# Performance work log

Hardware: AMD Instinct MI355X
Metric: run time of the kernel (lower is better)

The kernel has to match this reference:

```python
import jax, jax.numpy as jnp
import numpy as np

# db2 decomposition filters (pywt values); pytorch_wavelets reverses them and uses
# F.conv1d (cross-correlation), so we store the reversed filters.
_DEC_LO = np.array([-0.12940952255092145, 0.22414386804185735,
                    0.836516303737469, 0.48296291314469025])
_DEC_HI = np.array([-0.48296291314469025, 0.836516303737469,
                    -0.22414386804185735, 0.12940952255092145])
_H0 = jnp.asarray(_DEC_LO[::-1].copy(), dtype=jnp.float32)
_H1 = jnp.asarray(_DEC_HI[::-1].copy(), dtype=jnp.float32)


def _dwt_layer(x):
    """Vectorized equivalent of DWTLayer: db2 J=1 DWT along the channel axis at
    every (b,i,j) pixel, keeping first C//2 lo coeffs then first C//2 hi coeffs.
    pytorch_wavelets mode='zero' with L=4 and even C -> pad 2 each side, stride 2.
    x: [B, C, H, W] -> [B, C, H, W]
    """
    B, C, H, W = x.shape
    v = jnp.transpose(x, (0, 2, 3, 1)).reshape(B * H * W, 1, C)
    filt = jnp.stack([_H0, _H1])[:, None, :].astype(x.dtype)  # [2,1,4]
    out = jax.lax.conv_general_dilated(
        v, filt, window_strides=(2,), padding=((2, 2),),
        dimension_numbers=('NCH', 'OIH', 'NCH'))  # [BHW, 2, C//2 + 1]
    half = C // 2
    t = jnp.concatenate([out[:, 0, :half], out[:, 1, :half]], axis=-1)
    return jnp.transpose(t.reshape(B, H, W, C), (0, 3, 1, 2))


def setup_inputs() -> dict:
    key = jax.random.key(0)
    ks = jax.random.split(key, 7)
    B, C, H, W = 16, 360, 64, 64
    return {
        'x': jax.random.normal(ks[0], (B, C, H, W), dtype=jnp.float32),
        'conv_w': jax.random.normal(ks[1], (1, 1, 2, 7), dtype=jnp.float32) * 0.1,
        'conv_b': jax.random.normal(ks[2], (1,), dtype=jnp.float32) * 0.1,
        'w1': jax.random.normal(ks[3], (128, 90), dtype=jnp.float32) * 0.1,
        'b1': jax.random.normal(ks[4], (128,), dtype=jnp.float32) * 0.1,
        'w2': jax.random.normal(ks[5], (256, 128), dtype=jnp.float32) * 0.1,
        'b2': jax.random.normal(ks[6], (256,), dtype=jnp.float32) * 0.1,
    }


def reference(x, conv_w, conv_b, w1, b1, w2, b2):
    x = _dwt_layer(x)                     # [B,360,H,W]
    cd1 = x[:, 180:, :, :]                # detail half -> [B,180,H,W]
    cd1 = _dwt_layer(cd1)                 # [B,180,H,W]
    cd1 = cd1.reshape(-1, 1, 2, 90)       # torch .view(-1,2,90).unsqueeze(1)
    cd1 = jax.lax.conv_general_dilated(
        cd1, conv_w, window_strides=(1, 1), padding=((0, 0), (3, 3)),
        dimension_numbers=('NCHW', 'OIHW', 'NCHW'))
    cd1 = cd1 + conv_b[None, :, None, None]   # [N,1,1,90]
    cd1 = jax.nn.relu(cd1)
    cd1 = cd1.reshape(cd1.shape[0], 1, -1)    # [N,1,90]
    cd1 = jax.nn.relu(cd1 @ w1.T + b1)        # [N,1,128]
    out = cd1 @ w2.T + b2                     # [N,1,256]
    return out.reshape(-1, 256, 8, 8)
```

## Files before the change

kernel.cpp:

```cpp
#include <hip/hip_runtime.h>

using bf8   = __attribute__((ext_vector_type(8))) short;
using f32x4 = __attribute__((ext_vector_type(4))) float;

__device__ inline unsigned short f2bf(float f) {
  unsigned u = __float_as_uint(f);
  return (unsigned short)((u + 0x7FFFu + ((u >> 16) & 1u)) >> 16);
}
__device__ inline float bf2f(unsigned short h) {
  return __uint_as_float(((unsigned)h) << 16);
}

struct Gs { float g0[10]; float g1[10]; };
__host__ __device__ constexpr Gs make_g() {
  double H0[4] = {0.48296291314469025, 0.836516303737469,
                  0.22414386804185735, -0.12940952255092145};
  double H1[4] = {0.12940952255092145, -0.22414386804185735,
                  0.836516303737469, -0.48296291314469025};
  Gs r{};
  for (int d = 0; d < 10; ++d) {
    double a = 0.0, b = 0.0;
    for (int k = 0; k < 4; ++k) {
      int j = d - 2 * k;
      if (j >= 0 && j < 4) { a += H0[k] * H1[j]; b += H1[k] * H1[j]; }
    }
    r.g0[d] = (float)a; r.g1[d] = (float)b;
  }
  return r;
}

__global__ __launch_bounds__(256) void dwt2_kernel(const float* __restrict__ x,
                                                   unsigned short* __restrict__ A) {
  constexpr Gs G = make_g();
  const int bx    = blockIdx.x;
  const int seg   = bx & 7;
  const int pb    = bx >> 3;
  const int b     = pb >> 2;
  const int chunk = pb & 3;
  const int s     = chunk * 1024 + 4 * threadIdx.x;

  const float4* xb = (const float4*)(x + (size_t)b * 360 * 4096 + s);
  unsigned short* Ab = A + (size_t)b * 180 * 4096 + s;

  const int c0 = (seg * 90) >> 3;
  const int c1 = ((seg + 1) * 90) >> 3;

  float4 w[10];
  const int base = 4 * c0 - 6;
#pragma unroll
  for (int i = 0; i < 10; ++i) {
    const int idx = base + i;
    w[i] = (idx >= 0) ? xb[(size_t)idx * 1024] : float4{0.f, 0.f, 0.f, 0.f};
  }

  for (int c = c0; c < c1; ++c) {
    float4 nx[4];
    const bool pf = (c + 1 < c1);
    const int nb = 4 * c + 4;
#pragma unroll
    for (int i = 0; i < 4; ++i)
      nx[i] = pf ? xb[(size_t)(nb + i) * 1024] : float4{0.f, 0.f, 0.f, 0.f};

    float4 lo{0.f, 0.f, 0.f, 0.f}, hi{0.f, 0.f, 0.f, 0.f};
#pragma unroll
    for (int d = 0; d < 10; ++d) {
      lo.x = fmaf(G.g0[d], w[d].x, lo.x);
      lo.y = fmaf(G.g0[d], w[d].y, lo.y);
      lo.z = fmaf(G.g0[d], w[d].z, lo.z);
      lo.w = fmaf(G.g0[d], w[d].w, lo.w);
      hi.x = fmaf(G.g1[d], w[d].x, hi.x);
      hi.y = fmaf(G.g1[d], w[d].y, hi.y);
      hi.z = fmaf(G.g1[d], w[d].z, hi.z);
      hi.w = fmaf(G.g1[d], w[d].w, hi.w);
    }
    *(ushort4*)&Ab[(size_t)c * 4096] =
        ushort4{f2bf(lo.x), f2bf(lo.y), f2bf(lo.z), f2bf(lo.w)};
    *(ushort4*)&Ab[(size_t)(c + 90) * 4096] =
        ushort4{f2bf(hi.x), f2bf(hi.y), f2bf(hi.z), f2bf(hi.w)};
#pragma unroll
    for (int i = 0; i < 6; ++i) w[i] = w[i + 4];
#pragma unroll
    for (int i = 0; i < 4; ++i) w[6 + i] = nx[i];
  }
}

__global__ __launch_bounds__(256) void conv_kernel(
    const unsigned short* __restrict__ A,
    const float* __restrict__ cw, const float* __restrict__ cb,
    unsigned short* __restrict__ Y,
    const float* __restrict__ w1, const float* __restrict__ w2,
    unsigned short* __restrict__ w1b, unsigned short* __restrict__ w2b) {
  const int bx = blockIdx.x;
  if (bx >= 1024) {
    const int e = bx - 1024;
#pragma unroll
    for (int t = 0; t < 4; ++t) {
      const int i = e * 1024 + t * 256 + threadIdx.x;
      if (i < 13312) {
        const int o = i / 104, k = i - 104 * o;
        w1b[i] = (k < 90) ? f2bf(w1[o * 90 + k]) : (unsigned short)0;
      } else {
        const int j = i - 13312;
        const int o = j / 136, k = j - 136 * o;
        w2b[j] = (k < 128) ? f2bf(w2[o * 128 + k]) : (unsigned short)0;
      }
    }
    return;
  }

  __shared__ float As[64 * 180];
  const int tid = threadIdx.x;
  const size_t g0 = (size_t)bx * 64;

  const uint4* src = (const uint4*)(A + g0 * 180);
  for (int i = tid; i < 1440; i += 256) {
    uint4 v = src[i];
    float* d = &As[8 * i];
    d[0] = bf2f((unsigned short)(v.x & 0xFFFF));
    d[1] = bf2f((unsigned short)(v.x >> 16));
    d[2] = bf2f((unsigned short)(v.y & 0xFFFF));
    d[3] = bf2f((unsigned short)(v.y >> 16));
    d[4] = bf2f((unsigned short)(v.z & 0xFFFF));
    d[5] = bf2f((unsigned short)(v.z >> 16));
    d[6] = bf2f((unsigned short)(v.w & 0xFFFF));
    d[7] = bf2f((unsigned short)(v.w >> 16));
  }
  __syncthreads();

  float cwr[14];
#pragma unroll
  for (int k = 0; k < 14; ++k) cwr[k] = cw[k];
  const float cbv = cb[0];

  for (int i = tid; i < 64 * 24; i += 256) {
    const int g = i / 24, j4 = i - g * 24, j0 = 4 * j4;
    const float* Ag = &As[g * 180];
    float v0[10], v1[10];
#pragma unroll
    for (int t = 0; t < 10; ++t) {
      const int m = j0 - 3 + t;
      const bool ok = (m >= 0) && (m < 90);
      v0[t] = ok ? Ag[m] : 0.0f;
      v1[t] = ok ? Ag[90 + m] : 0.0f;
    }
    ushort4 o4;
    unsigned short* op = (unsigned short*)&o4;
#pragma unroll
    for (int d = 0; d < 4; ++d) {
      const int j = j0 + d;
      float acc = 0.0f;
      if (j < 90) {
        acc = cbv;
#pragma unroll
        for (int k = 0; k < 7; ++k) {
          acc = fmaf(v0[d + k], cwr[k], acc);
          acc = fmaf(v1[d + k], cwr[7 + k], acc);
        }
        acc = fmaxf(acc, 0.0f);
      }
      op[d] = f2bf(acc);
    }
    *(ushort4*)&Y[(g0 + g) * 96 + j0] = o4;
  }
}

__global__ __launch_bounds__(256) void mlp_mfma_kernel(
    const unsigned short* __restrict__ Y,
    const unsigned short* __restrict__ w1b,
    const unsigned short* __restrict__ w2b,
    const float* __restrict__ b1, const float* __restrict__ b2,
    float* __restrict__ out) {
  __shared__ unsigned short w1B[128 * 104];
  __shared__ unsigned short w2B[128 * 136];
  __shared__ unsigned short HY[64 * 136];
  __shared__ float bias[256];

  const int tid = threadIdx.x;
  const int fam = blockIdx.x & 1;
  const int cb  = blockIdx.x >> 1;

  {
    const uint4* s1 = (const uint4*)w1b;
    for (int i = tid; i < 1664; i += 256) ((uint4*)w1B)[i] = s1[i];
    const uint4* s2 = (const uint4*)(w2b + (size_t)fam * 128 * 136);
    for (int i = tid; i < 2176; i += 256) ((uint4*)w2B)[i] = s2[i];
    bias[tid] = (tid < 128) ? b1[tid] : b2[fam * 128 + (tid - 128)];
  }

  const int w = tid >> 6, lane = tid & 63;
  const int l15 = lane & 15, q = lane >> 4;
  const int mrow = 16 * w + l15;

  for (int it = 0; it < 4; ++it) {
    const size_t g0 = (size_t)(cb + 256 * it) * 64;

    __syncthreads();

    const uint4* ys = (const uint4*)(Y + g0 * 96);
    for (int i = tid; i < 768; i += 256) {
      const int r = i / 12, c = i - 12 * r;
      *(uint4*)&HY[r * 104 + 8 * c] = ys[i];
    }
    __syncthreads();

    bf8 ya[3];
#pragma unroll
    for (int ks = 0; ks < 3; ++ks)
      ya[ks] = *(const bf8*)&HY[mrow * 104 + 32 * ks + 8 * q];

    f32x4 acc1[8];
#pragma unroll
    for (int nt = 0; nt < 8; ++nt) {
      f32x4 a = {0.f, 0.f, 0.f, 0.f};
#pragma unroll
      for (int ks = 0; ks < 3; ++ks) {
        const bf8 wb = *(const bf8*)&w1B[(16 * nt + l15) * 104 + 32 * ks + 8 * q];
        a = __builtin_amdgcn_mfma_f32_16x16x32_bf16(ya[ks], wb, a, 0, 0, 0);
      }
      acc1[nt] = a;
    }
    __syncthreads();

#pragma unroll
    for (int nt = 0; nt < 8; ++nt) {
#pragma unroll
      for (int r = 0; r < 4; ++r) {
        const int n = 16 * w + 4 * q + r;
        const int o = 16 * nt + l15;
        HY[n * 136 + o] = f2bf(fmaxf(acc1[nt][r] + bias[o], 0.0f));
      }
    }
    __syncthreads();

    bf8 ha[4];
#pragma unroll
    for (int ks = 0; ks < 4; ++ks)
      ha[ks] = *(const bf8*)&HY[mrow * 136 + 32 * ks + 8 * q];

#pragma unroll 2
    for (int nt = 0; nt < 8; ++nt) {
      f32x4 a = {0.f, 0.f, 0.f, 0.f};
#pragma unroll
      for (int ks = 0; ks < 4; ++ks) {
        const bf8 wb = *(const bf8*)&w2B[(16 * nt + l15) * 136 + 32 * ks + 8 * q];
        a = __builtin_amdgcn_mfma_f32_16x16x32_bf16(ha[ks], wb, a, 0, 0, 0);
      }
#pragma unroll
      for (int r = 0; r < 4; ++r) {
        const int n = 16 * w + 4 * q + r;
        const int o = 16 * nt + l15;
        out[(g0 + n) * 256 + fam * 128 + o] = a[r] + bias[128 + o];
      }
    }
  }
}

extern "C" void kernel_launch(void* const* d_in, const int* in_sizes, int n_in,
                              void* d_out, int out_size, void* d_ws, size_t ws_size,
                              hipStream_t stream) {
  const float* x  = (const float*)d_in[0];
  const float* cw = (const float*)d_in[1];
  const float* cb = (const float*)d_in[2];
  const float* w1 = (const float*)d_in[3];
  const float* b1 = (const float*)d_in[4];
  const float* w2 = (const float*)d_in[5];
  const float* b2 = (const float*)d_in[6];
  float* outp = (float*)d_out;

  unsigned short* Abf = (unsigned short*)d_ws;
  unsigned short* Ybf = Abf + (size_t)16 * 180 * 4096;
  unsigned short* w1b = Ybf + (size_t)65536 * 96;
  unsigned short* w2b = w1b + 13312;

  dwt2_kernel<<<512, 256, 0, stream>>>(x, Abf);
  conv_kernel<<<1071, 256, 0, stream>>>(Abf, cw, cb, Ybf, w1, w2, w1b, w2b);
  mlp_mfma_kernel<<<512, 256, 0, stream>>>(Ybf, w1b, w2b, b1, b2, outp);
}
```

Before: 206.6 us.

## Fuse conv into MLP kernel and move weight conversion into DWT launch

Removes the separate conv kernel by computing the 2x7 conv+ReLU on the fly inside the MLP kernel, building MFMA A-fragments directly from bf16 DWT output staged in shared memory. Weight bf16 conversion moves into extra blocks of the DWT launch, so three launches become two and the Y intermediate buffer is no longer written or read. The MLP kernel now uses 512-thread blocks handling 128 rows, register-prefetches the next tile from global memory, and keeps biases in registers. The risks are higher register pressure, scalar bf16 LDS reads for the conv taps, and fewer blocks (256), which could lower occupancy.

```diff
diff --git a/kernel.cpp b/kernel.cpp
--- a/kernel.cpp
+++ b/kernel.cpp
@@ -30,9 +30,30 @@
 }
 
 __global__ __launch_bounds__(256) void dwt2_kernel(const float* __restrict__ x,
-                                                   unsigned short* __restrict__ A) {
+                                                   unsigned short* __restrict__ A,
+                                                   const float* __restrict__ w1,
+                                                   const float* __restrict__ w2,
+                                                   unsigned short* __restrict__ w1b,
+                                                   unsigned short* __restrict__ w2b) {
   constexpr Gs G = make_g();
-  const int bx    = blockIdx.x;
+  const int bx = blockIdx.x;
+  if (bx >= 512) {
+    const int e = bx - 512;
+#pragma unroll
+    for (int t = 0; t < 4; ++t) {
+      const int i = e * 1024 + t * 256 + threadIdx.x;
+      if (i < 13312) {
+        const int o = i / 104, k = i - 104 * o;
+        w1b[i] = (k < 90) ? f2bf(w1[o * 90 + k]) : (unsigned short)0;
+      } else {
+        const int j = i - 13312;
+        const int o = j / 136, k = j - 136 * o;
+        w2b[j] = (k < 128) ? f2bf(w2[o * 128 + k]) : (unsigned short)0;
+      }
+    }
+    return;
+  }
+
   const int seg   = bx & 7;
   const int pb    = bx >> 3;
   const int b     = pb >> 2;
@@ -84,129 +105,104 @@
   }
 }
 
-__global__ __launch_bounds__(256) void conv_kernel(
+__global__ __launch_bounds__(512, 1) void mlp_fused_kernel(
     const unsigned short* __restrict__ A,
-    const float* __restrict__ cw, const float* __restrict__ cb,
-    unsigned short* __restrict__ Y,
-    const float* __restrict__ w1, const float* __restrict__ w2,
-    unsigned short* __restrict__ w1b, unsigned short* __restrict__ w2b) {
-  const int bx = blockIdx.x;
-  if (bx >= 1024) {
-    const int e = bx - 1024;
-#pragma unroll
-    for (int t = 0; t < 4; ++t) {
-      const int i = e * 1024 + t * 256 + threadIdx.x;
-      if (i < 13312) {
-        const int o = i / 104, k = i - 104 * o;
-        w1b[i] = (k < 90) ? f2bf(w1[o * 90 + k]) : (unsigned short)0;
-      } else {
-        const int j = i - 13312;
-        const int o = j / 136, k = j - 136 * o;
-        w2b[j] = (k < 128) ? f2bf(w2[o * 128 + k]) : (unsigned short)0;
-      }
-    }
-    return;
-  }
-
-  __shared__ float As[64 * 180];
-  const int tid = threadIdx.x;
-  const size_t g0 = (size_t)bx * 64;
-
-  const uint4* src = (const uint4*)(A + g0 * 180);
-  for (int i = tid; i < 1440; i += 256) {
-    uint4 v = src[i];
-    float* d = &As[8 * i];
-    d[0] = bf2f((unsigned short)(v.x & 0xFFFF));
-    d[1] = bf2f((unsigned short)(v.x >> 16));
-    d[2] = bf2f((unsigned short)(v.y & 0xFFFF));
-    d[3] = bf2f((unsigned short)(v.y >> 16));
-    d[4] = bf2f((unsigned short)(v.z & 0xFFFF));
-    d[5] = bf2f((unsigned short)(v.z >> 16));
-    d[6] = bf2f((unsigned short)(v.w & 0xFFFF));
-    d[7] = bf2f((unsigned short)(v.w >> 16));
-  }
-  __syncthreads();
-
-  float cwr[14];
-#pragma unroll
-  for (int k = 0; k < 14; ++k) cwr[k] = cw[k];
-  const float cbv = cb[0];
-
-  for (int i = tid; i < 64 * 24; i += 256) {
-    const int g = i / 24, j4 = i - g * 24, j0 = 4 * j4;
-    const float* Ag = &As[g * 180];
-    float v0[10], v1[10];
-#pragma unroll
-    for (int t = 0; t < 10; ++t) {
-      const int m = j0 - 3 + t;
-      const bool ok = (m >= 0) && (m < 90);
-      v0[t] = ok ? Ag[m] : 0.0f;
-      v1[t] = ok ? Ag[90 + m] : 0.0f;
-    }
-    ushort4 o4;
-    unsigned short* op = (unsigned short*)&o4;
-#pragma unroll
-    for (int d = 0; d < 4; ++d) {
-      const int j = j0 + d;
-      float acc = 0.0f;
-      if (j < 90) {
-        acc = cbv;
-#pragma unroll
-        for (int k = 0; k < 7; ++k) {
-          acc = fmaf(v0[d + k], cwr[k], acc);
-          acc = fmaf(v1[d + k], cwr[7 + k], acc);
-        }
-        acc = fmaxf(acc, 0.0f);
-      }
-      op[d] = f2bf(acc);
-    }
-    *(ushort4*)&Y[(g0 + g) * 96 + j0] = o4;
-  }
-}
-
-__global__ __launch_bounds__(256) void mlp_mfma_kernel(
-    const unsigned short* __restrict__ Y,
+    const float* __restrict__ cw, const float* __restrict__ cbp,
     const unsigned short* __restrict__ w1b,
     const unsigned short* __restrict__ w2b,
     const float* __restrict__ b1, const float* __restrict__ b2,
     float* __restrict__ out) {
   __shared__ unsigned short w1B[128 * 104];
   __shared__ unsigned short w2B[128 * 136];
-  __shared__ unsigned short HY[64 * 136];
-  __shared__ float bias[256];
+  __shared__ unsigned short AsH[128 * 180];
 
   const int tid = threadIdx.x;
   const int fam = blockIdx.x & 1;
-  const int cb  = blockIdx.x >> 1;
+  const int cbk = blockIdx.x >> 1;
 
   {
     const uint4* s1 = (const uint4*)w1b;
-    for (int i = tid; i < 1664; i += 256) ((uint4*)w1B)[i] = s1[i];
+    for (int i = tid; i < 1664; i += 512) ((uint4*)w1B)[i] = s1[i];
     const uint4* s2 = (const uint4*)(w2b + (size_t)fam * 128 * 136);
-    for (int i = tid; i < 2176; i += 256) ((uint4*)w2B)[i] = s2[i];
-    bias[tid] = (tid < 128) ? b1[tid] : b2[fam * 128 + (tid - 128)];
-  }
+    for (int i = tid; i < 2176; i += 512) ((uint4*)w2B)[i] = s2[i];
+  }
+
+  float cwr[14];
+#pragma unroll
+  for (int k = 0; k < 14; ++k) cwr[k] = cw[k];
+  const float cbv = cbp[0];
 
   const int w = tid >> 6, lane = tid & 63;
   const int l15 = lane & 15, q = lane >> 4;
   const int mrow = 16 * w + l15;
 
+  float b1v[8], b2v[8];
+#pragma unroll
+  for (int nt = 0; nt < 8; ++nt) {
+    b1v[nt] = b1[16 * nt + l15];
+    b2v[nt] = b2[fam * 128 + 16 * nt + l15];
+  }
+
+  uint4 st[6];
+  {
+    const uint4* ns = (const uint4*)(A + (size_t)cbk * 128 * 180);
+#pragma unroll
+    for (int t = 0; t < 6; ++t) {
+      const int idx = tid + 512 * t;
+      if (idx < 2880) st[t] = ns[idx];
+    }
+  }
+
   for (int it = 0; it < 4; ++it) {
-    const size_t g0 = (size_t)(cb + 256 * it) * 64;
+    const size_t g0 = (size_t)(cbk + 128 * it) * 128;
 
     __syncthreads();
-
-    const uint4* ys = (const uint4*)(Y + g0 * 96);
-    for (int i = tid; i < 768; i += 256) {
-      const int r = i / 12, c = i - 12 * r;
-      *(uint4*)&HY[r * 104 + 8 * c] = ys[i];
+#pragma unroll
+    for (int t = 0; t < 6; ++t) {
+      const int idx = tid + 512 * t;
+      if (idx < 2880) ((uint4*)AsH)[idx] = st[t];
     }
     __syncthreads();
 
+    if (it < 3) {
+      const uint4* ns = (const uint4*)(A + (size_t)(cbk + 128 * (it + 1)) * 128 * 180);
+#pragma unroll
+      for (int t = 0; t < 6; ++t) {
+        const int idx = tid + 512 * t;
+        if (idx < 2880) st[t] = ns[idx];
+      }
+    }
+
     bf8 ya[3];
 #pragma unroll
-    for (int ks = 0; ks < 3; ++ks)
-      ya[ks] = *(const bf8*)&HY[mrow * 104 + 32 * ks + 8 * q];
+    for (int ks = 0; ks < 3; ++ks) {
+      const int j0 = 32 * ks + 8 * q;
+      float v0[14], v1[14];
+#pragma unroll
+      for (int t = 0; t < 14; ++t) {
+        const int m = j0 - 3 + t;
+        const bool ok = (m >= 0) && (m < 90);
+        v0[t] = ok ? bf2f(AsH[mrow * 180 + m]) : 0.0f;
+        v1[t] = ok ? bf2f(AsH[mrow * 180 + 90 + m]) : 0.0f;
+      }
+      bf8 r8;
+#pragma unroll
+      for (int d = 0; d < 8; ++d) {
+        const int j = j0 + d;
+        unsigned short rv = 0;
+        if (j < 90) {
+          float acc = cbv;
+#pragma unroll
+          for (int k = 0; k < 7; ++k) {
+            acc = fmaf(v0[d + k], cwr[k], acc);
+            acc = fmaf(v1[d + k], cwr[7 + k], acc);
+          }
+          rv = f2bf(fmaxf(acc, 0.0f));
+        }
+        r8[d] = (short)rv;
+      }
+      ya[ks] = r8;
+    }
 
     f32x4 acc1[8];
 #pragma unroll
@@ -227,15 +223,14 @@
       for (int r = 0; r < 4; ++r) {
         const int n = 16 * w + 4 * q + r;
         const int o = 16 * nt + l15;
-        HY[n * 136 + o] = f2bf(fmaxf(acc1[nt][r] + bias[o], 0.0f));
-      }
-    }
-    __syncthreads();
+        AsH[n * 136 + o] = f2bf(fmaxf(acc1[nt][r] + b1v[nt], 0.0f));
+      }
+    }
 
     bf8 ha[4];
 #pragma unroll
     for (int ks = 0; ks < 4; ++ks)
-      ha[ks] = *(const bf8*)&HY[mrow * 136 + 32 * ks + 8 * q];
+      ha[ks] = *(const bf8*)&AsH[mrow * 136 + 32 * ks + 8 * q];
 
 #pragma unroll 2
     for (int nt = 0; nt < 8; ++nt) {
@@ -248,8 +243,7 @@
 #pragma unroll
       for (int r = 0; r < 4; ++r) {
         const int n = 16 * w + 4 * q + r;
-        const int o = 16 * nt + l15;
-        out[(g0 + n) * 256 + fam * 128 + o] = a[r] + bias[128 + o];
+        out[(g0 + n) * 256 + fam * 128 + 16 * nt + l15] = a[r] + b2v[nt];
       }
     }
   }
@@ -268,11 +262,9 @@
   float* outp = (float*)d_out;
 
   unsigned short* Abf = (unsigned short*)d_ws;
-  unsigned short* Ybf = Abf + (size_t)16 * 180 * 4096;
-  unsigned short* w1b = Ybf + (size_t)65536 * 96;
+  unsigned short* w1b = Abf + (size_t)16 * 180 * 4096;
   unsigned short* w2b = w1b + 13312;
 
-  dwt2_kernel<<<512, 256, 0, stream>>>(x, Abf);
-  conv_kernel<<<1071, 256, 0, stream>>>(Abf, cw, cb, Ybf, w1, w2, w1b, w2b);
-  mlp_mfma_kernel<<<512, 256, 0, stream>>>(Ybf, w1b, w2b, b1, b2, outp);
-}
+  dwt2_kernel<<<559, 256, 0, stream>>>(x, Abf, w1, w2, w1b, w2b);
+  mlp_fused_kernel<<<256, 512, 0, stream>>>(Abf, cw, cb, w1b, w2b, b1, b2, outp);
+}
```

New measurement: 228.7 us. 1.11x slower.
